# Kernel tuning notes

Measured on AMD Instinct MI355X. Metric: run time of the kernel, lower is better.

The kernel has to match this reference:

```python
import jax, jax.numpy as jnp
import numpy as np

DIM = 4096
N_HEADS = 32
N_LOCAL_HEADS = 8
HEAD_DIM = 128
BATCH = 1
SEQLEN = 2048
ROPE_BASE = 10000.0


def setup_inputs() -> dict:
    key = jax.random.key(0)
    ks = jax.random.split(key, 6)
    x = jax.random.normal(ks[0], (BATCH, SEQLEN, DIM), dtype=jnp.float32)
    # RoPE freqs: [S, head_dim//2, 2] = (cos, sin)
    inv_freq = 1.0 / (ROPE_BASE ** (jnp.arange(0, HEAD_DIM, 2, dtype=jnp.float32) / HEAD_DIM))
    t = jnp.arange(SEQLEN, dtype=jnp.float32)
    freqs = jnp.outer(t, inv_freq)  # [S, head_dim//2]
    freqs_cis = jnp.stack([jnp.cos(freqs), jnp.sin(freqs)], axis=-1)  # [S, hd/2, 2]
    # causal additive mask [1, 1, S, S]
    neg = jnp.float32(-1e9)
    causal = jnp.tril(jnp.ones((SEQLEN, SEQLEN), dtype=bool))
    mask = jnp.where(causal, 0.0, neg)[None, None, :, :].astype(jnp.float32)
    s = 0.02
    wq = jax.random.normal(ks[1], (N_HEADS * HEAD_DIM, DIM), dtype=jnp.float32) * s
    wk = jax.random.normal(ks[2], (N_LOCAL_HEADS * HEAD_DIM, DIM), dtype=jnp.float32) * s
    wv = jax.random.normal(ks[3], (N_LOCAL_HEADS * HEAD_DIM, DIM), dtype=jnp.float32) * s
    wo = jax.random.normal(ks[4], (DIM, DIM), dtype=jnp.float32) * s
    return {"x": x, "freqs_cis": freqs_cis, "mask": mask,
            "wq": wq, "wk": wk, "wv": wv, "wo": wo}


def apply_rotary_emb(x, freqs_cis):
    # x: [B, S, H, head_dim]; freqs_cis: [S, head_dim//2, 2]
    B, S, H, hd = x.shape
    xs = x.reshape(B, S, H, hd // 2, 2)
    fc = freqs_cis[None, :, None, :, :]  # [1, S, 1, hd/2, 2]
    real = xs[..., 0] * fc[..., 0] - xs[..., 1] * fc[..., 1]
    imag = xs[..., 1] * fc[..., 0] + xs[..., 0] * fc[..., 1]
    return jnp.stack([real, imag], axis=-1).reshape(B, S, H, hd).astype(x.dtype)


def reference(x, freqs_cis, mask, wq, wk, wv, wo):
    B, S, _ = x.shape
    q = (x @ wq.T).reshape(B, S, N_HEADS, HEAD_DIM)
    k = (x @ wk.T).reshape(B, S, N_LOCAL_HEADS, HEAD_DIM)
    v = (x @ wv.T).reshape(B, S, N_LOCAL_HEADS, HEAD_DIM)
    q = apply_rotary_emb(q, freqs_cis)
    k = apply_rotary_emb(k, freqs_cis)
    # GQA: repeat_interleave kv heads to n_heads (done on head axis pre-transpose)
    rep = N_HEADS // N_LOCAL_HEADS
    k = jnp.repeat(k, rep, axis=2)
    v = jnp.repeat(v, rep, axis=2)
    # [B, H, S, hd]
    q, k, v = (t.transpose(0, 2, 1, 3) for t in (q, k, v))
    scale = 1.0 / jnp.sqrt(jnp.float32(HEAD_DIM))
    scores = jnp.einsum("bhqd,bhkd->bhqk", q, k) * scale + mask
    attn = jax.nn.softmax(scores, axis=-1)
    y = jnp.einsum("bhqk,bhkd->bhqd", attn, v)  # [B, H, S, hd]
    y = y.transpose(0, 2, 1, 3).reshape(B, S, N_HEADS * HEAD_DIM)
    return y @ wo.T
```

## Files before the change

kernel.cpp:

```cpp
#include <hip/hip_runtime.h>
#include <hip/hip_bf16.h>

typedef __bf16 bf16;
typedef __bf16 bf16x8 __attribute__((ext_vector_type(8)));
typedef float  f32x4  __attribute__((ext_vector_type(4)));

#define MFMA16(a,b,c) __builtin_amdgcn_mfma_f32_16x16x32_bf16(a,b,c,0,0,0)
#define KD 4096

__device__ __forceinline__ void gld_lds16(const void* g, void* l) {
    __builtin_amdgcn_global_load_lds(
        (const __attribute__((address_space(1))) unsigned int*)g,
        (__attribute__((address_space(3))) unsigned int*)l,
        16, 0, 0);
}

__global__ __launch_bounds__(256) void cast_bf16_kernel(const float* __restrict__ src,
                                                        bf16* __restrict__ dst, int n8) {
    int i = blockIdx.x * 256 + threadIdx.x;
    if (i >= n8) return;
    const float4* s4 = (const float4*)src;
    float4 a = s4[2*i], b = s4[2*i+1];
    bf16x8 o;
    o[0]=(bf16)a.x; o[1]=(bf16)a.y; o[2]=(bf16)a.z; o[3]=(bf16)a.w;
    o[4]=(bf16)b.x; o[5]=(bf16)b.y; o[6]=(bf16)b.z; o[7]=(bf16)b.w;
    ((bf16x8*)dst)[i] = o;
}

__global__ __launch_bounds__(256) void gemm_qkv(
    const bf16* __restrict__ A, const bf16* __restrict__ Wq,
    const bf16* __restrict__ Wk, const bf16* __restrict__ Wv,
    const float* __restrict__ freqs,
    bf16* __restrict__ qo, bf16* __restrict__ ko, bf16* __restrict__ vto)
{
    __shared__ bf16 As[128*32];
    __shared__ bf16 Bs[128*32];
    const int tid  = threadIdx.x;
    const int lane = tid & 63;
    const int w    = tid >> 6;
    const int wm = w & 1, wn = w >> 1;
    const int l15 = lane & 15, quad = lane >> 4;
    const int mBase = blockIdx.y * 128;
    const int nBase = blockIdx.x * 128;

    const bf16* bsrc;
    if (nBase < 4096)      bsrc = Wq + (size_t)nBase * KD;
    else if (nBase < 5120) bsrc = Wk + (size_t)(nBase - 4096) * KD;
    else                   bsrc = Wv + (size_t)(nBase - 5120) * KD;

    f32x4 acc[4][4];
    f32x4 zero = {0.f,0.f,0.f,0.f};
    #pragma unroll
    for (int i=0;i<4;i++)
        #pragma unroll
        for (int j=0;j<4;j++) acc[i][j] = zero;

    const int c0 = tid, c1 = tid + 256;
    const int r0 = c0 >> 2, o0 = (((c0 & 3) ^ ((r0 >> 1) & 3))) * 8;
    const int r1 = c1 >> 2, o1 = (((c1 & 3) ^ ((r1 >> 1) & 3))) * 8;
    const int akey = (l15 >> 1) & 3;

    for (int k0 = 0; k0 < KD; k0 += 32) {
        __syncthreads();
        gld_lds16(A + (size_t)(mBase + r0) * KD + k0 + o0, (char*)As + c0*16);
        gld_lds16(A + (size_t)(mBase + r1) * KD + k0 + o1, (char*)As + c1*16);
        gld_lds16(bsrc + (size_t)r0 * KD + k0 + o0, (char*)Bs + c0*16);
        gld_lds16(bsrc + (size_t)r1 * KD + k0 + o1, (char*)Bs + c1*16);
        __syncthreads();
        bf16x8 af[4], bfr[4];
        #pragma unroll
        for (int i=0;i<4;i++)
            af[i] = *(const bf16x8*)&As[(wm*64 + i*16 + l15)*32 + (quad ^ akey)*8];
        #pragma unroll
        for (int j=0;j<4;j++)
            bfr[j] = *(const bf16x8*)&Bs[(wn*64 + j*16 + l15)*32 + (quad ^ akey)*8];
        #pragma unroll
        for (int i=0;i<4;i++)
            #pragma unroll
            for (int j=0;j<4;j++)
                acc[i][j] = MFMA16(af[i], bfr[j], acc[i][j]);
    }

    const int region = (nBase < 4096) ? 0 : (nBase < 5120 ? 1 : 2);
    #pragma unroll
    for (int i=0;i<4;i++) {
        #pragma unroll
        for (int j=0;j<4;j++) {
            int col = nBase + wn*64 + j*16 + l15;
            #pragma unroll
            for (int r=0;r<4;r++) {
                int row = mBase + wm*64 + i*16 + quad*4 + r;
                float val = acc[i][j][r];
                if (region == 0) {
                    float partner = __shfl_xor(val, 1);
                    float2 cs = ((const float2*)freqs)[row*64 + ((col & 127) >> 1)];
                    float ov = (col & 1) ? (val * cs.x + partner * cs.y)
                                         : (val * cs.x - partner * cs.y);
                    qo[(size_t)row*4096 + col] = (bf16)(ov * 0.08838834764831845f);
                } else if (region == 1) {
                    float partner = __shfl_xor(val, 1);
                    int kc = col - 4096;
                    float2 cs = ((const float2*)freqs)[row*64 + ((kc & 127) >> 1)];
                    float ov = (kc & 1) ? (val * cs.x + partner * cs.y)
                                        : (val * cs.x - partner * cs.y);
                    ko[(size_t)row*1024 + kc] = (bf16)ov;
                } else {
                    int vc = col - 5120;
                    vto[(size_t)(vc >> 7)*262144 + (size_t)(vc & 127)*2048 + row] = (bf16)val;
                }
            }
        }
    }
}

__global__ __launch_bounds__(512, 4) void attn_kernel(
    const bf16* __restrict__ q, const bf16* __restrict__ k,
    const bf16* __restrict__ vt, bf16* __restrict__ y)
{
    __shared__ bf16 KsA[64*128], KsB[64*128];
    __shared__ bf16 VtsA[128*64], VtsB[128*64];
    __shared__ bf16 Ps[128*64];
    const int bid = blockIdx.x;
    const int kvh = bid & 7;
    const int h   = kvh*4 + ((bid >> 3) & 3);
    const int i16 = bid >> 5;
    const int qt  = (i16 < 8) ? (15 - 2*i16) : (2*i16 - 16);
    const int tid = threadIdx.x;
    const int lane = tid & 63;
    const int w    = tid >> 6;
    const int l15 = lane & 15, quad = lane >> 4;

    bf16x8 qf[4];
    const bf16* qp = q + (size_t)(qt*128 + w*16 + l15) * 4096 + h*128;
    #pragma unroll
    for (int ks=0;ks<4;ks++) qf[ks] = *(const bf16x8*)(qp + ks*32 + quad*8);

    f32x4 accO[8];
    f32x4 zero = {0.f,0.f,0.f,0.f};
    #pragma unroll
    for (int j=0;j<8;j++) accO[j] = zero;
    float l_r[4] = {0.f,0.f,0.f,0.f};

    const int nkt = 2 * (qt + 1);
    const bf16* kbase = k  + kvh*128;
    const bf16* vbase = vt + (size_t)kvh*262144;

    auto stage = [&](bf16* Ks, bf16* Vts, int kt) {
        const bf16* ksrc = kbase + (size_t)(kt*64) * 1024;
        const bf16* vsrc = vbase + kt*64;
        #pragma unroll
        for (int i=0;i<2;i++) {
            int c = tid + 512*i;
            int kr = c >> 4, kg = (c & 15) ^ (kr & 15);
            gld_lds16(ksrc + (size_t)kr*1024 + kg*8, (char*)Ks  + c*16);
            int vr = c >> 3, vg = (c & 7) ^ (vr & 7);
            gld_lds16(vsrc + (size_t)vr*2048 + vg*8, (char*)Vts + c*16);
        }
    };

    stage(KsA, VtsA, 0);
    for (int kt = 0; kt < nkt; kt++) {
        bf16* Ks  = (kt & 1) ? KsB  : KsA;
        bf16* Vts = (kt & 1) ? VtsB : VtsA;
        __syncthreads();
        if (kt + 1 < nkt) stage((kt & 1) ? KsA : KsB, (kt & 1) ? VtsA : VtsB, kt + 1);

        f32x4 Sf[4];
        #pragma unroll
        for (int j=0;j<4;j++) Sf[j] = zero;
        #pragma unroll
        for (int ks=0;ks<4;ks++) {
            #pragma unroll
            for (int j=0;j<4;j++) {
                bf16x8 kf = *(const bf16x8*)((const char*)Ks + (j*16+l15)*256
                                             + (((ks*4+quad) ^ l15))*16);
                Sf[j] = MFMA16(qf[ks], kf, Sf[j]);
            }
        }
        if (kt*64 + 63 > qt*128) {
            #pragma unroll
            for (int j=0;j<4;j++) {
                int kc = kt*64 + j*16 + l15;
                int qr0 = qt*128 + w*16 + quad*4;
                #pragma unroll
                for (int r=0;r<4;r++)
                    if (kc > qr0 + r) Sf[j][r] = -1e30f;
            }
        }

        #pragma unroll
        for (int j=0;j<4;j++) {
            int col = j*16 + l15;
            #pragma unroll
            for (int r=0;r<4;r++) {
                float e = __expf(Sf[j][r] - 12.0f);
                l_r[r] += e;
                int qr = w*16 + quad*4 + r;
                int ch = (col >> 3) ^ (qr & 7);
                *(bf16*)((char*)Ps + qr*128 + ch*16 + (col & 7)*2) = (bf16)e;
            }
        }
        #pragma unroll
        for (int ks=0;ks<2;ks++) {
            bf16x8 pf = *(const bf16x8*)((const char*)Ps + (w*16+l15)*128
                                         + (((ks*4+quad) ^ (l15 & 7)))*16);
            #pragma unroll
            for (int j=0;j<8;j++) {
                bf16x8 vf = *(const bf16x8*)((const char*)Vts + (j*16+l15)*128
                                             + (((ks*4+quad) ^ (l15 & 7)))*16);
                accO[j] = MFMA16(pf, vf, accO[j]);
            }
        }
    }
    float inv[4];
    #pragma unroll
    for (int r=0;r<4;r++) {
        float s = l_r[r];
        s += __shfl_xor(s, 1); s += __shfl_xor(s, 2);
        s += __shfl_xor(s, 4); s += __shfl_xor(s, 8);
        inv[r] = 1.0f / s;
    }
    #pragma unroll
    for (int j=0;j<8;j++) {
        int col = h*128 + j*16 + l15;
        #pragma unroll
        for (int r=0;r<4;r++) {
            int row = qt*128 + w*16 + quad*4 + r;
            y[(size_t)row*4096 + col] = (bf16)(accO[j][r] * inv[r]);
        }
    }
}

__global__ __launch_bounds__(256) void gemm_out(
    const bf16* __restrict__ A, const bf16* __restrict__ B, float* __restrict__ C)
{
    __shared__ bf16 As[128*32];
    __shared__ bf16 Bs[128*32];
    const int tid  = threadIdx.x;
    const int lane = tid & 63;
    const int w    = tid >> 6;
    const int wm = w & 1, wn = w >> 1;
    const int l15 = lane & 15, quad = lane >> 4;
    const int mBase = blockIdx.y * 128;
    const int nBase = blockIdx.x * 128;
    const bf16* bsrc = B + (size_t)nBase * KD;

    f32x4 acc[4][4];
    f32x4 zero = {0.f,0.f,0.f,0.f};
    #pragma unroll
    for (int i=0;i<4;i++)
        #pragma unroll
        for (int j=0;j<4;j++) acc[i][j] = zero;

    const int c0 = tid, c1 = tid + 256;
    const int r0 = c0 >> 2, o0 = (((c0 & 3) ^ ((r0 >> 1) & 3))) * 8;
    const int r1 = c1 >> 2, o1 = (((c1 & 3) ^ ((r1 >> 1) & 3))) * 8;
    const int akey = (l15 >> 1) & 3;

    for (int k0 = 0; k0 < KD; k0 += 32) {
        __syncthreads();
        gld_lds16(A + (size_t)(mBase + r0) * KD + k0 + o0, (char*)As + c0*16);
        gld_lds16(A + (size_t)(mBase + r1) * KD + k0 + o1, (char*)As + c1*16);
        gld_lds16(bsrc + (size_t)r0 * KD + k0 + o0, (char*)Bs + c0*16);
        gld_lds16(bsrc + (size_t)r1 * KD + k0 + o1, (char*)Bs + c1*16);
        __syncthreads();
        bf16x8 af[4], bfr[4];
        #pragma unroll
        for (int i=0;i<4;i++)
            af[i] = *(const bf16x8*)&As[(wm*64 + i*16 + l15)*32 + (quad ^ akey)*8];
        #pragma unroll
        for (int j=0;j<4;j++)
            bfr[j] = *(const bf16x8*)&Bs[(wn*64 + j*16 + l15)*32 + (quad ^ akey)*8];
        #pragma unroll
        for (int i=0;i<4;i++)
            #pragma unroll
            for (int j=0;j<4;j++)
                acc[i][j] = MFMA16(af[i], bfr[j], acc[i][j]);
    }
    #pragma unroll
    for (int i=0;i<4;i++)
        #pragma unroll
        for (int j=0;j<4;j++) {
            int col = nBase + wn*64 + j*16 + l15;
            #pragma unroll
            for (int r=0;r<4;r++) {
                int row = mBase + wm*64 + i*16 + quad*4 + r;
                C[(size_t)row*4096 + col] = acc[i][j][r];
            }
        }
}

extern "C" void kernel_launch(void* const* d_in, const int* in_sizes, int n_in,
                              void* d_out, int out_size, void* d_ws, size_t ws_size,
                              hipStream_t stream) {
    const float* x     = (const float*)d_in[0];
    const float* freqs = (const float*)d_in[1];
    const float* wq = (const float*)d_in[3];
    const float* wk = (const float*)d_in[4];
    const float* wv = (const float*)d_in[5];
    const float* wo = (const float*)d_in[6];
    float* out = (float*)d_out;

    bf16* xb  = (bf16*)d_ws;
    bf16* wqb = xb  + 8388608;
    bf16* wkb = wqb + 16777216;
    bf16* wvb = wkb + 4194304;
    bf16* qb  = wvb + 4194304;
    bf16* kb  = qb  + 8388608;
    bf16* vtb = kb  + 2097152;
    bf16* wob = wqb;
    bf16* yb  = xb;

    cast_bf16_kernel<<<4096, 256, 0, stream>>>(x,  xb,  1048576);
    cast_bf16_kernel<<<8192, 256, 0, stream>>>(wq, wqb, 2097152);
    cast_bf16_kernel<<<2048, 256, 0, stream>>>(wk, wkb, 524288);
    cast_bf16_kernel<<<2048, 256, 0, stream>>>(wv, wvb, 524288);
    gemm_qkv<<<dim3(48,16), 256, 0, stream>>>(xb, wqb, wkb, wvb, freqs, qb, kb, vtb);
    cast_bf16_kernel<<<8192, 256, 0, stream>>>(wo, wob, 2097152);
    attn_kernel<<<512, 512, 0, stream>>>(qb, kb, vtb, yb);
    gemm_out<<<dim3(32,16), 256, 0, stream>>>(yb, wob, out);
}
```

Before: 490.8 us.

## Rewrite QKV GEMM as 256x256 double-buffered pipelined kernel and fuse input casts

```diff
diff --git a/kernel.cpp b/kernel.cpp
--- a/kernel.cpp
+++ b/kernel.cpp
@@ -27,70 +27,186 @@
     ((bf16x8*)dst)[i] = o;
 }
 
-__global__ __launch_bounds__(256) void gemm_qkv(
+__global__ __launch_bounds__(256) void cast4_kernel(
+    const float* __restrict__ x,  const float* __restrict__ wq,
+    const float* __restrict__ wk, const float* __restrict__ wv,
+    bf16* __restrict__ xb, bf16* __restrict__ wqb,
+    bf16* __restrict__ wkb, bf16* __restrict__ wvb)
+{
+    int i = blockIdx.x * 256 + threadIdx.x;
+    const float* s; bf16* d; int off;
+    if (i < 1048576)      { s = x;  d = xb;  off = i; }
+    else if (i < 3145728) { s = wq; d = wqb; off = i - 1048576; }
+    else if (i < 3670016) { s = wk; d = wkb; off = i - 3145728; }
+    else                  { s = wv; d = wvb; off = i - 3670016; }
+    const float4* s4 = (const float4*)s;
+    float4 a = s4[2*off], b = s4[2*off+1];
+    bf16x8 o;
+    o[0]=(bf16)a.x; o[1]=(bf16)a.y; o[2]=(bf16)a.z; o[3]=(bf16)a.w;
+    o[4]=(bf16)b.x; o[5]=(bf16)b.y; o[6]=(bf16)b.z; o[7]=(bf16)b.w;
+    ((bf16x8*)d)[off] = o;
+}
+
+__global__ __launch_bounds__(512, 2) void gemm_qkv(
     const bf16* __restrict__ A, const bf16* __restrict__ Wq,
     const bf16* __restrict__ Wk, const bf16* __restrict__ Wv,
     const float* __restrict__ freqs,
     bf16* __restrict__ qo, bf16* __restrict__ ko, bf16* __restrict__ vto)
 {
-    __shared__ bf16 As[128*32];
-    __shared__ bf16 Bs[128*32];
+    __shared__ bf16 As[2*16384];
+    __shared__ bf16 Bs[2*16384];
     const int tid  = threadIdx.x;
     const int lane = tid & 63;
     const int w    = tid >> 6;
-    const int wm = w & 1, wn = w >> 1;
+    const int wm = w >> 2, wn = w & 3;
     const int l15 = lane & 15, quad = lane >> 4;
-    const int mBase = blockIdx.y * 128;
-    const int nBase = blockIdx.x * 128;
+
+    const int lin = blockIdx.x;
+    const int xcd = lin & 7, idx = lin >> 3;
+    const int bx = xcd*3 + idx % 3;
+    const int by = idx / 3;
+    const int mBase = by * 256;
+    const int nBase = bx * 256;
 
     const bf16* bsrc;
     if (nBase < 4096)      bsrc = Wq + (size_t)nBase * KD;
     else if (nBase < 5120) bsrc = Wk + (size_t)(nBase - 4096) * KD;
     else                   bsrc = Wv + (size_t)(nBase - 5120) * KD;
 
-    f32x4 acc[4][4];
+    const int l0 = tid, l1 = tid + 512;
+    const int rl0 = l0 >> 3, g0 = (l0 & 7) ^ (rl0 & 7);
+    const int rl1 = l1 >> 3, g1 = (l1 & 7) ^ (rl1 & 7);
+    const int arow0 = rl0 + (rl0 & 64);
+    const int arow1 = rl1 + (rl1 & 64);
+    const int brow0 = ((rl0 >> 5) << 6) + (rl0 & 31);
+    const int brow1 = ((rl1 >> 5) << 6) + (rl1 & 31);
+
+    auto stageA = [&](int pp, int half, int t) {
+        gld_lds16(A + (size_t)(mBase + half*64 + arow0)*KD + t*64 + g0*8,
+                  (char*)As + (pp*16384 + half*8192)*2 + l0*16);
+        gld_lds16(A + (size_t)(mBase + half*64 + arow1)*KD + t*64 + g1*8,
+                  (char*)As + (pp*16384 + half*8192)*2 + l1*16);
+    };
+    auto stageB = [&](int pp, int half, int t) {
+        gld_lds16(bsrc + (size_t)(brow0 + half*32)*KD + t*64 + g0*8,
+                  (char*)Bs + (pp*16384 + half*8192)*2 + l0*16);
+        gld_lds16(bsrc + (size_t)(brow1 + half*32)*KD + t*64 + g1*8,
+                  (char*)Bs + (pp*16384 + half*8192)*2 + l1*16);
+    };
+
+    const int sA  = (wm*64 + l15) * 64;
+    const int sB  = (wn*32 + l15) * 64;
+    const int k0s = ((quad)     ^ (l15 & 7)) * 8;
+    const int k1s = ((4 + quad) ^ (l15 & 7)) * 8;
+
+    f32x4 acc[8][4];
     f32x4 zero = {0.f,0.f,0.f,0.f};
     #pragma unroll
-    for (int i=0;i<4;i++)
+    for (int i=0;i<8;i++)
         #pragma unroll
         for (int j=0;j<4;j++) acc[i][j] = zero;
 
-    const int c0 = tid, c1 = tid + 256;
-    const int r0 = c0 >> 2, o0 = (((c0 & 3) ^ ((r0 >> 1) & 3))) * 8;
-    const int r1 = c1 >> 2, o1 = (((c1 & 3) ^ ((r1 >> 1) & 3))) * 8;
-    const int akey = (l15 >> 1) & 3;
-
-    for (int k0 = 0; k0 < KD; k0 += 32) {
-        __syncthreads();
-        gld_lds16(A + (size_t)(mBase + r0) * KD + k0 + o0, (char*)As + c0*16);
-        gld_lds16(A + (size_t)(mBase + r1) * KD + k0 + o1, (char*)As + c1*16);
-        gld_lds16(bsrc + (size_t)r0 * KD + k0 + o0, (char*)Bs + c0*16);
-        gld_lds16(bsrc + (size_t)r1 * KD + k0 + o1, (char*)Bs + c1*16);
-        __syncthreads();
-        bf16x8 af[4], bfr[4];
-        #pragma unroll
-        for (int i=0;i<4;i++)
-            af[i] = *(const bf16x8*)&As[(wm*64 + i*16 + l15)*32 + (quad ^ akey)*8];
-        #pragma unroll
-        for (int j=0;j<4;j++)
-            bfr[j] = *(const bf16x8*)&Bs[(wn*64 + j*16 + l15)*32 + (quad ^ akey)*8];
-        #pragma unroll
-        for (int i=0;i<4;i++)
-            #pragma unroll
-            for (int j=0;j<4;j++)
-                acc[i][j] = MFMA16(af[i], bfr[j], acc[i][j]);
+    bf16x8 a_[4][2], b0_[2][2], b1_[2][2];
+
+    stageA(0, 0, 0);
+    stageB(0, 0, 0);
+    stageB(0, 1, 0);
+    stageA(0, 1, 0);
+    asm volatile("s_waitcnt vmcnt(4)" ::: "memory");
+    __builtin_amdgcn_s_barrier();
+
+    for (int t = 0; t < 64; ++t) {
+        const int p = t & 1, np = p ^ 1, pb = p * 16384;
+        const bool nl = (t < 63);
+
+        #pragma unroll
+        for (int i=0;i<4;i++) {
+            a_[i][0] = *(const bf16x8*)&As[pb + sA + i*1024 + k0s];
+            a_[i][1] = *(const bf16x8*)&As[pb + sA + i*1024 + k1s];
+        }
+        #pragma unroll
+        for (int j=0;j<2;j++) {
+            b0_[j][0] = *(const bf16x8*)&Bs[pb + sB + j*1024 + k0s];
+            b0_[j][1] = *(const bf16x8*)&Bs[pb + sB + j*1024 + k1s];
+        }
+        if (nl) { stageA(np, 0, t+1); asm volatile("s_waitcnt vmcnt(4)" ::: "memory"); }
+        else    {                     asm volatile("s_waitcnt vmcnt(2)" ::: "memory"); }
+        __builtin_amdgcn_s_barrier();
+        asm volatile("s_waitcnt lgkmcnt(0)" ::: "memory");
+        __builtin_amdgcn_s_setprio(1);
+        #pragma unroll
+        for (int i=0;i<4;i++)
+            #pragma unroll
+            for (int j=0;j<2;j++) {
+                acc[i][j] = MFMA16(a_[i][0], b0_[j][0], acc[i][j]);
+                acc[i][j] = MFMA16(a_[i][1], b0_[j][1], acc[i][j]);
+            }
+        __builtin_amdgcn_s_setprio(0);
+        __builtin_amdgcn_s_barrier();
+
+        #pragma unroll
+        for (int j=0;j<2;j++) {
+            b1_[j][0] = *(const bf16x8*)&Bs[pb + 8192 + sB + j*1024 + k0s];
+            b1_[j][1] = *(const bf16x8*)&Bs[pb + 8192 + sB + j*1024 + k1s];
+        }
+        if (nl) { stageB(np, 0, t+1); asm volatile("s_waitcnt vmcnt(4)" ::: "memory"); }
+        else    {                     asm volatile("s_waitcnt vmcnt(0)" ::: "memory"); }
+        __builtin_amdgcn_s_barrier();
+        asm volatile("s_waitcnt lgkmcnt(0)" ::: "memory");
+        __builtin_amdgcn_s_setprio(1);
+        #pragma unroll
+        for (int i=0;i<4;i++)
+            #pragma unroll
+            for (int j=0;j<2;j++) {
+                acc[i][2+j] = MFMA16(a_[i][0], b1_[j][0], acc[i][2+j]);
+                acc[i][2+j] = MFMA16(a_[i][1], b1_[j][1], acc[i][2+j]);
+            }
+        __builtin_amdgcn_s_setprio(0);
+        __builtin_amdgcn_s_barrier();
+
+        #pragma unroll
+        for (int i=0;i<4;i++) {
+            a_[i][0] = *(const bf16x8*)&As[pb + 8192 + sA + i*1024 + k0s];
+            a_[i][1] = *(const bf16x8*)&As[pb + 8192 + sA + i*1024 + k1s];
+        }
+        if (nl) stageB(np, 1, t+1);
+        __builtin_amdgcn_s_barrier();
+        asm volatile("s_waitcnt lgkmcnt(0)" ::: "memory");
+        __builtin_amdgcn_s_setprio(1);
+        #pragma unroll
+        for (int i=0;i<4;i++)
+            #pragma unroll
+            for (int j=0;j<2;j++) {
+                acc[4+i][2+j] = MFMA16(a_[i][0], b1_[j][0], acc[4+i][2+j]);
+                acc[4+i][2+j] = MFMA16(a_[i][1], b1_[j][1], acc[4+i][2+j]);
+            }
+        __builtin_amdgcn_s_setprio(0);
+        __builtin_amdgcn_s_barrier();
+
+        if (nl) { stageA(np, 1, t+1); asm volatile("s_waitcnt vmcnt(4)" ::: "memory"); }
+        __builtin_amdgcn_s_barrier();
+        __builtin_amdgcn_s_setprio(1);
+        #pragma unroll
+        for (int i=0;i<4;i++)
+            #pragma unroll
+            for (int j=0;j<2;j++) {
+                acc[4+i][j] = MFMA16(a_[i][0], b0_[j][0], acc[4+i][j]);
+                acc[4+i][j] = MFMA16(a_[i][1], b0_[j][1], acc[4+i][j]);
+            }
+        __builtin_amdgcn_s_setprio(0);
+        __builtin_amdgcn_s_barrier();
     }
 
     const int region = (nBase < 4096) ? 0 : (nBase < 5120 ? 1 : 2);
     #pragma unroll
-    for (int i=0;i<4;i++) {
-        #pragma unroll
-        for (int j=0;j<4;j++) {
-            int col = nBase + wn*64 + j*16 + l15;
+    for (int ai=0; ai<8; ai++) {
+        #pragma unroll
+        for (int bj=0; bj<4; bj++) {
+            int col = nBase + wn*64 + bj*16 + l15;
             #pragma unroll
             for (int r=0;r<4;r++) {
-                int row = mBase + wm*64 + i*16 + quad*4 + r;
-                float val = acc[i][j][r];
+                int row = mBase + wm*128 + ai*16 + quad*4 + r;
+                float val = acc[ai][bj][r];
                 if (region == 0) {
                     float partner = __shfl_xor(val, 1);
                     float2 cs = ((const float2*)freqs)[row*64 + ((col & 127) >> 1)];
@@ -311,11 +427,8 @@
     bf16* wob = wqb;
     bf16* yb  = xb;
 
-    cast_bf16_kernel<<<4096, 256, 0, stream>>>(x,  xb,  1048576);
-    cast_bf16_kernel<<<8192, 256, 0, stream>>>(wq, wqb, 2097152);
-    cast_bf16_kernel<<<2048, 256, 0, stream>>>(wk, wkb, 524288);
-    cast_bf16_kernel<<<2048, 256, 0, stream>>>(wv, wvb, 524288);
-    gemm_qkv<<<dim3(48,16), 256, 0, stream>>>(xb, wqb, wkb, wvb, freqs, qb, kb, vtb);
+    cast4_kernel<<<16384, 256, 0, stream>>>(x, wq, wk, wv, xb, wqb, wkb, wvb);
+    gemm_qkv<<<192, 512, 0, stream>>>(xb, wqb, wkb, wvb, freqs, qb, kb, vtb);
     cast_bf16_kernel<<<8192, 256, 0, stream>>>(wo, wob, 2097152);
     attn_kernel<<<512, 512, 0, stream>>>(qb, kb, vtb, yb);
     gemm_out<<<dim3(32,16), 256, 0, stream>>>(yb, wob, out);
```

Result: no change. 500.1 us (+1.9%).

## Give each attention warp two query sub-tiles and fuse the four input casts

Applied to the files above, without the earlier changes.

```diff
diff --git a/kernel.cpp b/kernel.cpp
--- a/kernel.cpp
+++ b/kernel.cpp
@@ -25,6 +25,26 @@
     o[0]=(bf16)a.x; o[1]=(bf16)a.y; o[2]=(bf16)a.z; o[3]=(bf16)a.w;
     o[4]=(bf16)b.x; o[5]=(bf16)b.y; o[6]=(bf16)b.z; o[7]=(bf16)b.w;
     ((bf16x8*)dst)[i] = o;
+}
+
+__global__ __launch_bounds__(256) void cast4_kernel(
+    const float* __restrict__ x,  const float* __restrict__ wq,
+    const float* __restrict__ wk, const float* __restrict__ wv,
+    bf16* __restrict__ xb, bf16* __restrict__ wqb,
+    bf16* __restrict__ wkb, bf16* __restrict__ wvb)
+{
+    int i = blockIdx.x * 256 + threadIdx.x;
+    const float* s; bf16* d; int off;
+    if (i < 1048576)      { s = x;  d = xb;  off = i; }
+    else if (i < 3145728) { s = wq; d = wqb; off = i - 1048576; }
+    else if (i < 3670016) { s = wk; d = wkb; off = i - 3145728; }
+    else                  { s = wv; d = wvb; off = i - 3670016; }
+    const float4* s4 = (const float4*)s;
+    float4 a = s4[2*off], b = s4[2*off+1];
+    bf16x8 o;
+    o[0]=(bf16)a.x; o[1]=(bf16)a.y; o[2]=(bf16)a.z; o[3]=(bf16)a.w;
+    o[4]=(bf16)b.x; o[5]=(bf16)b.y; o[6]=(bf16)b.z; o[7]=(bf16)b.w;
+    ((bf16x8*)d)[off] = o;
 }
 
 __global__ __launch_bounds__(256) void gemm_qkv(
@@ -113,7 +133,7 @@
     }
 }
 
-__global__ __launch_bounds__(512, 4) void attn_kernel(
+__global__ __launch_bounds__(256, 2) void attn_kernel(
     const bf16* __restrict__ q, const bf16* __restrict__ k,
     const bf16* __restrict__ vt, bf16* __restrict__ y)
 {
@@ -130,16 +150,21 @@
     const int w    = tid >> 6;
     const int l15 = lane & 15, quad = lane >> 4;
 
-    bf16x8 qf[4];
-    const bf16* qp = q + (size_t)(qt*128 + w*16 + l15) * 4096 + h*128;
-    #pragma unroll
-    for (int ks=0;ks<4;ks++) qf[ks] = *(const bf16x8*)(qp + ks*32 + quad*8);
-
-    f32x4 accO[8];
+    bf16x8 qf[2][4];
+    #pragma unroll
+    for (int i=0;i<2;i++) {
+        const bf16* qp = q + (size_t)(qt*128 + w*32 + i*16 + l15) * 4096 + h*128;
+        #pragma unroll
+        for (int ks=0;ks<4;ks++) qf[i][ks] = *(const bf16x8*)(qp + ks*32 + quad*8);
+    }
+
+    f32x4 accO[2][8];
     f32x4 zero = {0.f,0.f,0.f,0.f};
     #pragma unroll
-    for (int j=0;j<8;j++) accO[j] = zero;
-    float l_r[4] = {0.f,0.f,0.f,0.f};
+    for (int i=0;i<2;i++)
+        #pragma unroll
+        for (int j=0;j<8;j++) accO[i][j] = zero;
+    float l_r[2][4] = {{0.f,0.f,0.f,0.f},{0.f,0.f,0.f,0.f}};
 
     const int nkt = 2 * (qt + 1);
     const bf16* kbase = k  + kvh*128;
@@ -149,8 +174,8 @@
         const bf16* ksrc = kbase + (size_t)(kt*64) * 1024;
         const bf16* vsrc = vbase + kt*64;
         #pragma unroll
-        for (int i=0;i<2;i++) {
-            int c = tid + 512*i;
+        for (int i=0;i<4;i++) {
+            int c = tid + 256*i;
             int kr = c >> 4, kg = (c & 15) ^ (kr & 15);
             gld_lds16(ksrc + (size_t)kr*1024 + kg*8, (char*)Ks  + c*16);
             int vr = c >> 3, vg = (c & 7) ^ (vr & 7);
@@ -165,68 +190,83 @@
         __syncthreads();
         if (kt + 1 < nkt) stage((kt & 1) ? KsA : KsB, (kt & 1) ? VtsA : VtsB, kt + 1);
 
-        f32x4 Sf[4];
-        #pragma unroll
-        for (int j=0;j<4;j++) Sf[j] = zero;
+        f32x4 Sf[2][4];
+        #pragma unroll
+        for (int i=0;i<2;i++)
+            #pragma unroll
+            for (int j=0;j<4;j++) Sf[i][j] = zero;
         #pragma unroll
         for (int ks=0;ks<4;ks++) {
             #pragma unroll
             for (int j=0;j<4;j++) {
                 bf16x8 kf = *(const bf16x8*)((const char*)Ks + (j*16+l15)*256
                                              + (((ks*4+quad) ^ l15))*16);
-                Sf[j] = MFMA16(qf[ks], kf, Sf[j]);
+                Sf[0][j] = MFMA16(qf[0][ks], kf, Sf[0][j]);
+                Sf[1][j] = MFMA16(qf[1][ks], kf, Sf[1][j]);
             }
         }
         if (kt*64 + 63 > qt*128) {
             #pragma unroll
+            for (int i=0;i<2;i++) {
+                int qr0 = qt*128 + w*32 + i*16 + quad*4;
+                #pragma unroll
+                for (int j=0;j<4;j++) {
+                    int kc = kt*64 + j*16 + l15;
+                    #pragma unroll
+                    for (int r=0;r<4;r++)
+                        if (kc > qr0 + r) Sf[i][j][r] = -1e30f;
+                }
+            }
+        }
+
+        #pragma unroll
+        for (int i=0;i<2;i++) {
+            #pragma unroll
             for (int j=0;j<4;j++) {
-                int kc = kt*64 + j*16 + l15;
-                int qr0 = qt*128 + w*16 + quad*4;
+                int col = j*16 + l15;
                 #pragma unroll
-                for (int r=0;r<4;r++)
-                    if (kc > qr0 + r) Sf[j][r] = -1e30f;
-            }
-        }
-
-        #pragma unroll
-        for (int j=0;j<4;j++) {
-            int col = j*16 + l15;
-            #pragma unroll
-            for (int r=0;r<4;r++) {
-                float e = __expf(Sf[j][r] - 12.0f);
-                l_r[r] += e;
-                int qr = w*16 + quad*4 + r;
-                int ch = (col >> 3) ^ (qr & 7);
-                *(bf16*)((char*)Ps + qr*128 + ch*16 + (col & 7)*2) = (bf16)e;
+                for (int r=0;r<4;r++) {
+                    float e = __expf(Sf[i][j][r] - 12.0f);
+                    l_r[i][r] += e;
+                    int qr = w*32 + i*16 + quad*4 + r;
+                    int ch = (col >> 3) ^ (qr & 7);
+                    *(bf16*)((char*)Ps + qr*128 + ch*16 + (col & 7)*2) = (bf16)e;
+                }
             }
         }
         #pragma unroll
         for (int ks=0;ks<2;ks++) {
-            bf16x8 pf = *(const bf16x8*)((const char*)Ps + (w*16+l15)*128
-                                         + (((ks*4+quad) ^ (l15 & 7)))*16);
+            bf16x8 pf0 = *(const bf16x8*)((const char*)Ps + (w*32+l15)*128
+                                          + (((ks*4+quad) ^ (l15 & 7)))*16);
+            bf16x8 pf1 = *(const bf16x8*)((const char*)Ps + (w*32+16+l15)*128
+                                          + (((ks*4+quad) ^ (l15 & 7)))*16);
             #pragma unroll
             for (int j=0;j<8;j++) {
                 bf16x8 vf = *(const bf16x8*)((const char*)Vts + (j*16+l15)*128
                                              + (((ks*4+quad) ^ (l15 & 7)))*16);
-                accO[j] = MFMA16(pf, vf, accO[j]);
-            }
-        }
-    }
-    float inv[4];
-    #pragma unroll
-    for (int r=0;r<4;r++) {
-        float s = l_r[r];
-        s += __shfl_xor(s, 1); s += __shfl_xor(s, 2);
-        s += __shfl_xor(s, 4); s += __shfl_xor(s, 8);
-        inv[r] = 1.0f / s;
-    }
-    #pragma unroll
-    for (int j=0;j<8;j++) {
-        int col = h*128 + j*16 + l15;
+                accO[0][j] = MFMA16(pf0, vf, accO[0][j]);
+                accO[1][j] = MFMA16(pf1, vf, accO[1][j]);
+            }
+        }
+    }
+    #pragma unroll
+    for (int i=0;i<2;i++) {
+        float inv[4];
         #pragma unroll
         for (int r=0;r<4;r++) {
-            int row = qt*128 + w*16 + quad*4 + r;
-            y[(size_t)row*4096 + col] = (bf16)(accO[j][r] * inv[r]);
+            float s = l_r[i][r];
+            s += __shfl_xor(s, 1); s += __shfl_xor(s, 2);
+            s += __shfl_xor(s, 4); s += __shfl_xor(s, 8);
+            inv[r] = 1.0f / s;
+        }
+        #pragma unroll
+        for (int j=0;j<8;j++) {
+            int col = h*128 + j*16 + l15;
+            #pragma unroll
+            for (int r=0;r<4;r++) {
+                int row = qt*128 + w*32 + i*16 + quad*4 + r;
+                y[(size_t)row*4096 + col] = (bf16)(accO[i][j][r] * inv[r]);
+            }
         }
     }
 }
@@ -311,12 +351,9 @@
     bf16* wob = wqb;
     bf16* yb  = xb;
 
-    cast_bf16_kernel<<<4096, 256, 0, stream>>>(x,  xb,  1048576);
-    cast_bf16_kernel<<<8192, 256, 0, stream>>>(wq, wqb, 2097152);
-    cast_bf16_kernel<<<2048, 256, 0, stream>>>(wk, wkb, 524288);
-    cast_bf16_kernel<<<2048, 256, 0, stream>>>(wv, wvb, 524288);
+    cast4_kernel<<<16384, 256, 0, stream>>>(x, wq, wk, wv, xb, wqb, wkb, wvb);
     gemm_qkv<<<dim3(48,16), 256, 0, stream>>>(xb, wqb, wkb, wvb, freqs, qb, kb, vtb);
     cast_bf16_kernel<<<8192, 256, 0, stream>>>(wo, wob, 2097152);
-    attn_kernel<<<512, 512, 0, stream>>>(qb, kb, vtb, yb);
+    attn_kernel<<<512, 256, 0, stream>>>(qb, kb, vtb, yb);
     gemm_out<<<dim3(32,16), 256, 0, stream>>>(yb, wob, out);
 }
```

Result: slower. 510.1 us (+3.9%).

## Halve GEMM M-tile to 64 and fuse weight casts into one launch

Applied to the files above, without the earlier changes.

```diff
diff --git a/kernel.cpp b/kernel.cpp
--- a/kernel.cpp
+++ b/kernel.cpp
@@ -27,20 +27,63 @@
     ((bf16x8*)dst)[i] = o;
 }
 
+__global__ __launch_bounds__(256) void cast4_kernel(
+    const float* __restrict__ x,  const float* __restrict__ wq,
+    const float* __restrict__ wk, const float* __restrict__ wv,
+    bf16* __restrict__ xb, bf16* __restrict__ wqb,
+    bf16* __restrict__ wkb, bf16* __restrict__ wvb)
+{
+    int i = blockIdx.x * 256 + threadIdx.x;
+    const float* s; bf16* d; int off;
+    if (i < 1048576)      { s = x;  d = xb;  off = i; }
+    else if (i < 3145728) { s = wq; d = wqb; off = i - 1048576; }
+    else if (i < 3670016) { s = wk; d = wkb; off = i - 3145728; }
+    else                  { s = wv; d = wvb; off = i - 3670016; }
+    const float4* s4 = (const float4*)s;
+    float4 a = s4[2*off], b = s4[2*off+1];
+    bf16x8 o;
+    o[0]=(bf16)a.x; o[1]=(bf16)a.y; o[2]=(bf16)a.z; o[3]=(bf16)a.w;
+    o[4]=(bf16)b.x; o[5]=(bf16)b.y; o[6]=(bf16)b.z; o[7]=(bf16)b.w;
+    ((bf16x8*)d)[off] = o;
+}
+
+__global__ __launch_bounds__(256) void cast5_kernel(
+    const float* __restrict__ x,  const float* __restrict__ wq,
+    const float* __restrict__ wk, const float* __restrict__ wv,
+    const float* __restrict__ wo,
+    bf16* __restrict__ xb, bf16* __restrict__ wqb,
+    bf16* __restrict__ wkb, bf16* __restrict__ wvb,
+    bf16* __restrict__ wob)
+{
+    int i = blockIdx.x * 256 + threadIdx.x;
+    const float* s; bf16* d; int off;
+    if (i < 1048576)      { s = x;  d = xb;  off = i; }
+    else if (i < 3145728) { s = wq; d = wqb; off = i - 1048576; }
+    else if (i < 3670016) { s = wk; d = wkb; off = i - 3145728; }
+    else if (i < 4194304) { s = wv; d = wvb; off = i - 3670016; }
+    else                  { s = wo; d = wob; off = i - 4194304; }
+    const float4* s4 = (const float4*)s;
+    float4 a = s4[2*off], b = s4[2*off+1];
+    bf16x8 o;
+    o[0]=(bf16)a.x; o[1]=(bf16)a.y; o[2]=(bf16)a.z; o[3]=(bf16)a.w;
+    o[4]=(bf16)b.x; o[5]=(bf16)b.y; o[6]=(bf16)b.z; o[7]=(bf16)b.w;
+    ((bf16x8*)d)[off] = o;
+}
+
 __global__ __launch_bounds__(256) void gemm_qkv(
     const bf16* __restrict__ A, const bf16* __restrict__ Wq,
     const bf16* __restrict__ Wk, const bf16* __restrict__ Wv,
     const float* __restrict__ freqs,
     bf16* __restrict__ qo, bf16* __restrict__ ko, bf16* __restrict__ vto)
 {
-    __shared__ bf16 As[128*32];
+    __shared__ bf16 As[64*32];
     __shared__ bf16 Bs[128*32];
     const int tid  = threadIdx.x;
     const int lane = tid & 63;
     const int w    = tid >> 6;
     const int wm = w & 1, wn = w >> 1;
     const int l15 = lane & 15, quad = lane >> 4;
-    const int mBase = blockIdx.y * 128;
+    const int mBase = blockIdx.y * 64;
     const int nBase = blockIdx.x * 128;
 
     const bf16* bsrc;
@@ -48,10 +91,10 @@
     else if (nBase < 5120) bsrc = Wk + (size_t)(nBase - 4096) * KD;
     else                   bsrc = Wv + (size_t)(nBase - 5120) * KD;
 
-    f32x4 acc[4][4];
+    f32x4 acc[2][4];
     f32x4 zero = {0.f,0.f,0.f,0.f};
     #pragma unroll
-    for (int i=0;i<4;i++)
+    for (int i=0;i<2;i++)
         #pragma unroll
         for (int j=0;j<4;j++) acc[i][j] = zero;
 
@@ -63,19 +106,18 @@
     for (int k0 = 0; k0 < KD; k0 += 32) {
         __syncthreads();
         gld_lds16(A + (size_t)(mBase + r0) * KD + k0 + o0, (char*)As + c0*16);
-        gld_lds16(A + (size_t)(mBase + r1) * KD + k0 + o1, (char*)As + c1*16);
         gld_lds16(bsrc + (size_t)r0 * KD + k0 + o0, (char*)Bs + c0*16);
         gld_lds16(bsrc + (size_t)r1 * KD + k0 + o1, (char*)Bs + c1*16);
         __syncthreads();
-        bf16x8 af[4], bfr[4];
-        #pragma unroll
-        for (int i=0;i<4;i++)
-            af[i] = *(const bf16x8*)&As[(wm*64 + i*16 + l15)*32 + (quad ^ akey)*8];
+        bf16x8 af[2], bfr[4];
+        #pragma unroll
+        for (int i=0;i<2;i++)
+            af[i] = *(const bf16x8*)&As[(wm*32 + i*16 + l15)*32 + (quad ^ akey)*8];
         #pragma unroll
         for (int j=0;j<4;j++)
             bfr[j] = *(const bf16x8*)&Bs[(wn*64 + j*16 + l15)*32 + (quad ^ akey)*8];
         #pragma unroll
-        for (int i=0;i<4;i++)
+        for (int i=0;i<2;i++)
             #pragma unroll
             for (int j=0;j<4;j++)
                 acc[i][j] = MFMA16(af[i], bfr[j], acc[i][j]);
@@ -83,13 +125,13 @@
 
     const int region = (nBase < 4096) ? 0 : (nBase < 5120 ? 1 : 2);
     #pragma unroll
-    for (int i=0;i<4;i++) {
+    for (int i=0;i<2;i++) {
         #pragma unroll
         for (int j=0;j<4;j++) {
             int col = nBase + wn*64 + j*16 + l15;
             #pragma unroll
             for (int r=0;r<4;r++) {
-                int row = mBase + wm*64 + i*16 + quad*4 + r;
+                int row = mBase + wm*32 + i*16 + quad*4 + r;
                 float val = acc[i][j][r];
                 if (region == 0) {
                     float partner = __shfl_xor(val, 1);
@@ -234,21 +276,21 @@
 __global__ __launch_bounds__(256) void gemm_out(
     const bf16* __restrict__ A, const bf16* __restrict__ B, float* __restrict__ C)
 {
-    __shared__ bf16 As[128*32];
+    __shared__ bf16 As[64*32];
     __shared__ bf16 Bs[128*32];
     const int tid  = threadIdx.x;
     const int lane = tid & 63;
     const int w    = tid >> 6;
     const int wm = w & 1, wn = w >> 1;
     const int l15 = lane & 15, quad = lane >> 4;
-    const int mBase = blockIdx.y * 128;
+    const int mBase = blockIdx.y * 64;
     const int nBase = blockIdx.x * 128;
     const bf16* bsrc = B + (size_t)nBase * KD;
 
-    f32x4 acc[4][4];
+    f32x4 acc[2][4];
     f32x4 zero = {0.f,0.f,0.f,0.f};
     #pragma unroll
-    for (int i=0;i<4;i++)
+    for (int i=0;i<2;i++)
         #pragma unroll
         for (int j=0;j<4;j++) acc[i][j] = zero;
 
@@ -260,31 +302,30 @@
     for (int k0 = 0; k0 < KD; k0 += 32) {
         __syncthreads();
         gld_lds16(A + (size_t)(mBase + r0) * KD + k0 + o0, (char*)As + c0*16);
-        gld_lds16(A + (size_t)(mBase + r1) * KD + k0 + o1, (char*)As + c1*16);
         gld_lds16(bsrc + (size_t)r0 * KD + k0 + o0, (char*)Bs + c0*16);
         gld_lds16(bsrc + (size_t)r1 * KD + k0 + o1, (char*)Bs + c1*16);
         __syncthreads();
-        bf16x8 af[4], bfr[4];
-        #pragma unroll
-        for (int i=0;i<4;i++)
-            af[i] = *(const bf16x8*)&As[(wm*64 + i*16 + l15)*32 + (quad ^ akey)*8];
+        bf16x8 af[2], bfr[4];
+        #pragma unroll
+        for (int i=0;i<2;i++)
+            af[i] = *(const bf16x8*)&As[(wm*32 + i*16 + l15)*32 + (quad ^ akey)*8];
         #pragma unroll
         for (int j=0;j<4;j++)
             bfr[j] = *(const bf16x8*)&Bs[(wn*64 + j*16 + l15)*32 + (quad ^ akey)*8];
         #pragma unroll
-        for (int i=0;i<4;i++)
+        for (int i=0;i<2;i++)
             #pragma unroll
             for (int j=0;j<4;j++)
                 acc[i][j] = MFMA16(af[i], bfr[j], acc[i][j]);
     }
     #pragma unroll
-    for (int i=0;i<4;i++)
+    for (int i=0;i<2;i++)
         #pragma unroll
         for (int j=0;j<4;j++) {
             int col = nBase + wn*64 + j*16 + l15;
             #pragma unroll
             for (int r=0;r<4;r++) {
-                int row = mBase + wm*64 + i*16 + quad*4 + r;
+                int row = mBase + wm*32 + i*16 + quad*4 + r;
                 C[(size_t)row*4096 + col] = acc[i][j][r];
             }
         }
@@ -308,15 +349,21 @@
     bf16* qb  = wvb + 4194304;
     bf16* kb  = qb  + 8388608;
     bf16* vtb = kb  + 2097152;
-    bf16* wob = wqb;
     bf16* yb  = xb;
 
-    cast_bf16_kernel<<<4096, 256, 0, stream>>>(x,  xb,  1048576);
-    cast_bf16_kernel<<<8192, 256, 0, stream>>>(wq, wqb, 2097152);
-    cast_bf16_kernel<<<2048, 256, 0, stream>>>(wk, wkb, 524288);
-    cast_bf16_kernel<<<2048, 256, 0, stream>>>(wv, wvb, 524288);
-    gemm_qkv<<<dim3(48,16), 256, 0, stream>>>(xb, wqb, wkb, wvb, freqs, qb, kb, vtb);
-    cast_bf16_kernel<<<8192, 256, 0, stream>>>(wo, wob, 2097152);
-    attn_kernel<<<512, 512, 0, stream>>>(qb, kb, vtb, yb);
-    gemm_out<<<dim3(32,16), 256, 0, stream>>>(yb, wob, out);
-}
+    const size_t need_sep = (size_t)(46137344 + 16777216) * sizeof(bf16);
+    if (ws_size >= need_sep) {
+        bf16* wob = vtb + 2097152;
+        cast5_kernel<<<24576, 256, 0, stream>>>(x, wq, wk, wv, wo, xb, wqb, wkb, wvb, wob);
+        gemm_qkv<<<dim3(48,32), 256, 0, stream>>>(xb, wqb, wkb, wvb, freqs, qb, kb, vtb);
+        attn_kernel<<<512, 512, 0, stream>>>(qb, kb, vtb, yb);
+        gemm_out<<<dim3(32,32), 256, 0, stream>>>(yb, wob, out);
+    } else {
+        bf16* wob = wqb;
+        cast4_kernel<<<16384, 256, 0, stream>>>(x, wq, wk, wv, xb, wqb, wkb, wvb);
+        gemm_qkv<<<dim3(48,32), 256, 0, stream>>>(xb, wqb, wkb, wvb, freqs, qb, kb, vtb);
+        cast_bf16_kernel<<<8192, 256, 0, stream>>>(wo, wob, 2097152);
+        attn_kernel<<<512, 512, 0, stream>>>(qb, kb, vtb, yb);
+        gemm_out<<<dim3(32,32), 256, 0, stream>>>(yb, wob, out);
+    }
+}
```

New measurement: 559.1 us. +13.9%, slower.
